# Performance work log

Hardware: AMD Instinct MI355X
Metric: run time of the kernel (lower is better)

Reference implementation:

```python
import jax, jax.numpy as jnp
import numpy as np

D = 512       # d_model
H = 8         # n_heads
L = 6         # n_blocks
DFF = 2048    # d_ffn
IN_DIM = 4096
OUT_DIM = 1000
B = 8
S = 512
DK = D // H
EPS = 1e-5
NEG = -1e9    # masked_fill value from source (-1000000000.0)

# sinusoidal positional encoding table (matches Positional_Encoding)
_pos = np.arange(5000)[:, None].astype(np.float64)
_div = np.exp(np.arange(0, D, 2) * (-np.log(10000.0) / D))
_pe = np.zeros((5000, D), np.float32)
_pe[:, 0::2] = np.sin(_pos * _div)
_pe[:, 1::2] = np.cos(_pos * _div)
PE = jnp.asarray(_pe)


def _ln(x, g, b):
    m = jnp.mean(x, -1, keepdims=True)
    v = jnp.var(x, -1, keepdims=True)
    return (x - m) * jax.lax.rsqrt(v + EPS) * g + b


def _attn(q, k, v, causal):
    # q:[B,Sq,D], k/v:[B,Sk,D] -> multi-head attention with source's quirky mask
    b, sq, _ = q.shape
    sk = k.shape[1]
    q = q.reshape(b, sq, H, DK).transpose(0, 2, 1, 3)
    k = k.reshape(b, sk, H, DK).transpose(0, 2, 1, 3)
    v = v.reshape(b, sk, H, DK).transpose(0, 2, 1, 3)
    s = jnp.einsum('bhqd,bhkd->bhqk', q, k) / jnp.sqrt(jnp.asarray(DK, q.dtype))
    mask = s != 0.0  # faithful: source masks positions where score == padding (0)
    if causal:
        mask = mask & jnp.tril(jnp.ones((sq, sk), bool))
    s = jnp.where(mask, s, NEG)
    p = jax.nn.softmax(s, axis=-1)
    o = jnp.einsum('bhqk,bhkd->bhqd', p, v)
    return o.transpose(0, 2, 1, 3).reshape(b, sq, D)


def _ffn(x, w1, b1, w2, b2):
    return jax.nn.relu(x @ w1 + b1) @ w2 + b2


def setup_inputs() -> dict:
    key = jax.random.key(0)
    ks = iter(jax.random.split(key, 40))

    def w(shape, s=0.02):
        return jax.random.normal(next(ks), shape, jnp.float32) * s

    inp = {}
    inp['x'] = jax.random.randint(next(ks), (B, S), 0, IN_DIM)
    inp['target'] = jax.random.randint(next(ks), (B,), 0, OUT_DIM)
    inp['in_emb'] = w((IN_DIM, D), 1.0)
    inp['out_emb'] = w((OUT_DIM, D), 1.0)
    # encoder params (stacked over layers)
    inp['enc_qkv_w'] = w((L, 3, D, D))
    inp['enc_qkv_b'] = w((L, 3, D))
    inp['enc_ln1_g'] = jnp.ones((L, D), jnp.float32)
    inp['enc_ln1_b'] = jnp.zeros((L, D), jnp.float32)
    inp['enc_ffn1_w'] = w((L, D, DFF))
    inp['enc_ffn1_b'] = w((L, DFF))
    inp['enc_ffn2_w'] = w((L, DFF, D))
    inp['enc_ffn2_b'] = w((L, D))
    inp['enc_ln2_g'] = jnp.ones((L, D), jnp.float32)
    inp['enc_ln2_b'] = jnp.zeros((L, D), jnp.float32)
    # decoder params
    inp['dec_qkv1_w'] = w((L, 3, D, D))
    inp['dec_qkv1_b'] = w((L, 3, D))
    inp['dec_ln1_g'] = jnp.ones((L, D), jnp.float32)
    inp['dec_ln1_b'] = jnp.zeros((L, D), jnp.float32)
    inp['dec_qkv2_w'] = w((L, 3, D, D))
    inp['dec_qkv2_b'] = w((L, 3, D))
    inp['dec_ln2_g'] = jnp.ones((L, D), jnp.float32)
    inp['dec_ln2_b'] = jnp.zeros((L, D), jnp.float32)
    inp['dec_ffn1_w'] = w((L, D, DFF))
    inp['dec_ffn1_b'] = w((L, DFF))
    inp['dec_ffn2_w'] = w((L, DFF, D))
    inp['dec_ffn2_b'] = w((L, D))
    inp['dec_ln3_g'] = jnp.ones((L, D), jnp.float32)
    inp['dec_ln3_b'] = jnp.zeros((L, D), jnp.float32)
    inp['out_w'] = w((D, OUT_DIM))
    inp['out_b'] = w((OUT_DIM,))
    return inp


def reference(x, target, in_emb, out_emb,
              enc_qkv_w, enc_qkv_b, enc_ln1_g, enc_ln1_b,
              enc_ffn1_w, enc_ffn1_b, enc_ffn2_w, enc_ffn2_b,
              enc_ln2_g, enc_ln2_b,
              dec_qkv1_w, dec_qkv1_b, dec_ln1_g, dec_ln1_b,
              dec_qkv2_w, dec_qkv2_b, dec_ln2_g, dec_ln2_b,
              dec_ffn1_w, dec_ffn1_b, dec_ffn2_w, dec_ffn2_b,
              dec_ln3_g, dec_ln3_b, out_w, out_b):
    scale = jnp.sqrt(jnp.float32(D))
    # encoder: embed tokens + positional encoding (dropout is identity at eval)
    e = in_emb[x] * scale + PE[None, :S]
    for i in range(L):
        q = e @ enc_qkv_w[i, 0] + enc_qkv_b[i, 0]
        k = e @ enc_qkv_w[i, 1] + enc_qkv_b[i, 1]
        v = e @ enc_qkv_w[i, 2] + enc_qkv_b[i, 2]
        e = _ln(_attn(q, k, v, False) + e, enc_ln1_g[i], enc_ln1_b[i])
        e = _ln(e + _ffn(e, enc_ffn1_w[i], enc_ffn1_b[i], enc_ffn2_w[i], enc_ffn2_b[i]),
                enc_ln2_g[i], enc_ln2_b[i])
    # decoder: target.unsqueeze(1) -> seq len 1
    d = out_emb[target][:, None, :] * scale + PE[None, :1]
    for i in range(L):
        q = d @ dec_qkv1_w[i, 0] + dec_qkv1_b[i, 0]
        k = d @ dec_qkv1_w[i, 1] + dec_qkv1_b[i, 1]
        v = d @ dec_qkv1_w[i, 2] + dec_qkv1_b[i, 2]
        d = _ln(_attn(q, k, v, True) + d, dec_ln1_g[i], dec_ln1_b[i])
        q = d @ dec_qkv2_w[i, 0] + dec_qkv2_b[i, 0]
        k = e @ dec_qkv2_w[i, 1] + dec_qkv2_b[i, 1]
        v = e @ dec_qkv2_w[i, 2] + dec_qkv2_b[i, 2]
        d = _ln(_attn(q, k, v, False) + d, dec_ln2_g[i], dec_ln2_b[i])
        d = _ln(d + _ffn(d, dec_ffn1_w[i], dec_ffn1_b[i], dec_ffn2_w[i], dec_ffn2_b[i]),
                dec_ln3_g[i], dec_ln3_b[i])
    return d @ out_w + out_b  # [B, 1, OUT_DIM] logits (source never applies its softmax)
```

## Files before the change

kernel.cpp:

```cpp
#include <hip/hip_runtime.h>
#include <hip/hip_bf16.h>

#define DM 512
#define NH 8
#define DK 64
#define SEQ 512
#define NB 8
#define NL 6
#define DFF 2048
#define OUTD 1000
#define EMB_SCALE 22.627416997969522f
#define PE_C (-0.017988946039015984)

typedef __bf16 bf16x8 __attribute__((ext_vector_type(8)));
typedef __bf16 bf16x4 __attribute__((ext_vector_type(4)));
typedef float f32x4 __attribute__((ext_vector_type(4)));

__device__ __forceinline__ void load16_lds(const __bf16* g, __bf16* l) {
  __builtin_amdgcn_global_load_lds(
      (const __attribute__((address_space(1))) void*)g,
      (__attribute__((address_space(3))) void*)l, 16, 0, 0);
}

__device__ __forceinline__ float dot8(bf16x8 w, const float* a) {
  float s = 0.f;
#pragma unroll
  for (int j = 0; j < 8; ++j) s += (float)w[j] * a[j];
  return s;
}

__global__ __launch_bounds__(256) void pe_kernel(float* __restrict__ pe) {
  int s = blockIdx.x;
  int d2 = threadIdx.x;
  double div = exp((double)(2 * d2) * PE_C);
  double arg = (double)s * div;
  pe[(size_t)s * DM + 2 * d2] = (float)sin(arg);
  pe[(size_t)s * DM + 2 * d2 + 1] = (float)cos(arg);
}

__global__ __launch_bounds__(256) void embed_enc(const int* __restrict__ x,
                                                 const float* __restrict__ emb,
                                                 const float* __restrict__ pe,
                                                 float* __restrict__ e,
                                                 __bf16* __restrict__ eb) {
  int idx = blockIdx.x * 256 + threadIdx.x;
  int d = idx & (DM - 1);
  int bs = idx >> 9;
  int s = bs & (SEQ - 1);
  int tok = x[bs];
  float v = emb[(size_t)tok * DM + d] * EMB_SCALE + pe[(size_t)s * DM + d];
  e[idx] = v;
  eb[idx] = (__bf16)v;
}

__global__ __launch_bounds__(256) void embed_dec(const int* __restrict__ t,
                                                 const float* __restrict__ emb,
                                                 float* __restrict__ dd) {
  int idx = blockIdx.x * 256 + threadIdx.x;
  int d = idx & (DM - 1);
  int b = idx >> 9;
  float pe = (d & 1) ? 1.0f : 0.0f;
  dd[idx] = emb[(size_t)t[b] * DM + d] * EMB_SCALE + pe;
}

__global__ __launch_bounds__(256) void transpose_w(const float* __restrict__ W,
                                                   __bf16* __restrict__ WT,
                                                   int K, int N) {
  __shared__ float t[32][33];
  size_t off = (size_t)blockIdx.z * K * N;
  W += off; WT += off;
  int k0 = blockIdx.y * 32, n0 = blockIdx.x * 32;
  int tx = threadIdx.x & 7, ty = threadIdx.x >> 3;
  float4 v = *(const float4*)&W[(size_t)(k0 + ty) * N + n0 + tx * 4];
  t[ty][tx * 4 + 0] = v.x; t[ty][tx * 4 + 1] = v.y;
  t[ty][tx * 4 + 2] = v.z; t[ty][tx * 4 + 3] = v.w;
  __syncthreads();
  bf16x4 o;
  o[0] = (__bf16)t[tx * 4 + 0][ty];
  o[1] = (__bf16)t[tx * 4 + 1][ty];
  o[2] = (__bf16)t[tx * 4 + 2][ty];
  o[3] = (__bf16)t[tx * 4 + 3][ty];
  *(bf16x4*)&WT[(size_t)(n0 + ty) * K + k0 + tx * 4] = o;
}

__global__ __launch_bounds__(256) void transpose_ow(const float* __restrict__ W,
                                                    __bf16* __restrict__ WT) {
  __shared__ float t[32][33];
  int n0 = blockIdx.x * 32, k0 = blockIdx.y * 32;
  int tid = threadIdx.x;
  for (int i = tid; i < 1024; i += 256) {
    int kk = i >> 5, nn = i & 31;
    t[kk][nn] = (n0 + nn < OUTD) ? W[(size_t)(k0 + kk) * OUTD + n0 + nn] : 0.f;
  }
  __syncthreads();
  for (int i = tid; i < 1024; i += 256) {
    int nn = i >> 5, kk = i & 31;
    if (n0 + nn < OUTD)
      WT[(size_t)(n0 + nn) * DM + k0 + kk] = (__bf16)t[kk][nn];
  }
}

template <int BN, bool RELU, bool WF32, bool WBF16, bool TRV, bool KVM>
__global__ __launch_bounds__(256) void mfma_gemm(
    const __bf16* __restrict__ A, const __bf16* __restrict__ BT,
    const float* __restrict__ bias, float* __restrict__ C,
    __bf16* __restrict__ Cb, __bf16* __restrict__ Vt, int M, int N, int K,
    long btStride, long bStride, long cStride) {
  int z = blockIdx.z;
  if (KVM) {
    long idx = (long)(z >> 1) * 3 + 1 + (z & 1);
    BT += idx * btStride;
    bias += idx * bStride;
  } else {
    BT += (size_t)z * btStride;
    bias += (size_t)z * bStride;
  }
  if (WF32) C += (size_t)z * cStride;
  if (WBF16) Cb += (size_t)z * cStride;

  constexpr int NI = BN / 32;
  __shared__ __bf16 As[128 * 64];
  __shared__ __bf16 Bs[BN * 64];

  int tid = threadIdx.x;
  int wave = tid >> 6, lane = tid & 63;
  int wm = wave >> 1, wn = wave & 1;
  int quad = lane >> 4, l16 = lane & 15;
  int rlane = lane >> 3, c8 = lane & 7;
  int m0 = blockIdx.y * 128, n0 = blockIdx.x * BN;
  int gcol = ((c8 ^ rlane) * 8);

  f32x4 acc[4][NI];
#pragma unroll
  for (int i = 0; i < 4; ++i)
#pragma unroll
    for (int j = 0; j < NI; ++j) acc[i][j] = (f32x4){0.f, 0.f, 0.f, 0.f};

  for (int k0 = 0; k0 < K; k0 += 64) {
    __syncthreads();
#pragma unroll
    for (int j = 0; j < 4; ++j) {
      int row = j * 32 + wave * 8 + rlane;
      load16_lds(&A[(size_t)(m0 + row) * K + k0 + gcol],
                 &As[(j * 32 + wave * 8) * 64]);
    }
#pragma unroll
    for (int j = 0; j < BN / 32; ++j) {
      int row = j * 32 + wave * 8 + rlane;
      load16_lds(&BT[(size_t)(n0 + row) * K + k0 + gcol],
                 &Bs[(j * 32 + wave * 8) * 64]);
    }
    __syncthreads();
#pragma unroll
    for (int kk = 0; kk < 64; kk += 32) {
      bf16x8 af[4], bf[NI];
#pragma unroll
      for (int i = 0; i < 4; ++i) {
        int row = wm * 64 + i * 16 + l16;
        af[i] = *(const bf16x8*)&As[row * 64 + ((((kk >> 3) + quad) ^ (row & 7)) * 8)];
      }
#pragma unroll
      for (int i = 0; i < NI; ++i) {
        int row = wn * (BN / 2) + i * 16 + l16;
        bf[i] = *(const bf16x8*)&Bs[row * 64 + ((((kk >> 3) + quad) ^ (row & 7)) * 8)];
      }
#pragma unroll
      for (int mi = 0; mi < 4; ++mi)
#pragma unroll
        for (int ni = 0; ni < NI; ++ni)
          acc[mi][ni] = __builtin_amdgcn_mfma_f32_16x16x32_bf16(
              af[mi], bf[ni], acc[mi][ni], 0, 0, 0);
    }
  }

#pragma unroll
  for (int ni = 0; ni < NI; ++ni) {
    int col = n0 + wn * (BN / 2) + ni * 16 + l16;
    float bv = bias[col];
    if (TRV && z == 2) {
      int b = m0 >> 9;
#pragma unroll
      for (int mi = 0; mi < 4; ++mi) {
        int srow = (m0 & 511) + wm * 64 + mi * 16 + quad * 4;
        bf16x4 pk;
#pragma unroll
        for (int r = 0; r < 4; ++r) pk[r] = (__bf16)(acc[mi][ni][r] + bv);
        *(bf16x4*)&Vt[((size_t)(b * 512 + col)) * 512 + srow] = pk;
      }
    } else {
#pragma unroll
      for (int mi = 0; mi < 4; ++mi) {
#pragma unroll
        for (int r = 0; r < 4; ++r) {
          int row = m0 + wm * 64 + mi * 16 + quad * 4 + r;
          float v = acc[mi][ni][r] + bv;
          if (RELU) v = fmaxf(v, 0.f);
          if (WF32) C[(size_t)row * N + col] = v;
          if (WBF16) Cb[(size_t)row * N + col] = (__bf16)v;
        }
      }
    }
  }
}

#define SCP 520
__global__ __launch_bounds__(256) void attn_mfma(const __bf16* __restrict__ QKV,
                                                 const __bf16* __restrict__ Vt,
                                                 float* __restrict__ O) {
  __shared__ __bf16 Sc[16 * SCP];
  __shared__ __bf16 Tt[64 * 64];

  const long ACTL = (long)NB * SEQ * DM;
  int tid = threadIdx.x;
  int wave = tid >> 6, lane = tid & 63;
  int quad = lane >> 4, l16 = lane & 15;
  int rlane = lane >> 3, c8 = lane & 7;
  int q0 = blockIdx.x * 16;
  int bh = blockIdx.y, b = bh >> 3, h = bh & 7;
  const __bf16* Q = QKV;
  const __bf16* Kp = QKV + ACTL;
  size_t baseQ = ((size_t)b * SEQ + q0) * DM + h * DK;
  size_t baseK = ((size_t)b * SEQ) * DM + h * DK;
  const __bf16* VtB = Vt + ((size_t)(b * 512 + h * 64)) * 512;
  int gcol = (c8 ^ rlane) * 8;

  bf16x8 af0 = *(const bf16x8*)&Q[baseQ + (size_t)l16 * DM + quad * 8];
  bf16x8 af1 = *(const bf16x8*)&Q[baseQ + (size_t)l16 * DM + 32 + quad * 8];

  for (int kt = 0; kt < 8; ++kt) {
    __syncthreads();
#pragma unroll
    for (int j = 0; j < 2; ++j) {
      int row = j * 32 + wave * 8 + rlane;
      load16_lds(&Kp[baseK + (size_t)(kt * 64 + row) * DM + gcol],
                 &Tt[(j * 32 + wave * 8) * 64]);
    }
    __syncthreads();
    f32x4 acc = (f32x4){0.f, 0.f, 0.f, 0.f};
    int krow = wave * 16 + l16, sw = krow & 7;
    bf16x8 b0 = *(const bf16x8*)&Tt[krow * 64 + ((quad ^ sw) * 8)];
    bf16x8 b1 = *(const bf16x8*)&Tt[krow * 64 + (((4 + quad) ^ sw) * 8)];
    acc = __builtin_amdgcn_mfma_f32_16x16x32_bf16(af0, b0, acc, 0, 0, 0);
    acc = __builtin_amdgcn_mfma_f32_16x16x32_bf16(af1, b1, acc, 0, 0, 0);
#pragma unroll
    for (int r = 0; r < 4; ++r)
      Sc[(quad * 4 + r) * SCP + kt * 64 + wave * 16 + l16] =
          (__bf16)(acc[r] * 0.125f);
  }
  __syncthreads();

#pragma unroll
  for (int rr = 0; rr < 4; ++rr) {
    int r = wave * 4 + rr;
    float v[8];
    float mx = -1e30f;
#pragma unroll
    for (int j = 0; j < 8; ++j) {
      v[j] = (float)Sc[r * SCP + j * 64 + lane];
      mx = fmaxf(mx, v[j]);
    }
    for (int o = 32; o > 0; o >>= 1) mx = fmaxf(mx, __shfl_xor(mx, o));
    float sum = 0.f;
#pragma unroll
    for (int j = 0; j < 8; ++j) { v[j] = __expf(v[j] - mx); sum += v[j]; }
    for (int o = 32; o > 0; o >>= 1) sum += __shfl_xor(sum, o);
    float inv = 1.f / sum;
#pragma unroll
    for (int j = 0; j < 8; ++j)
      Sc[r * SCP + j * 64 + lane] = (__bf16)(v[j] * inv);
  }

  f32x4 oacc = (f32x4){0.f, 0.f, 0.f, 0.f};
  for (int kt = 0; kt < 8; ++kt) {
    __syncthreads();
#pragma unroll
    for (int j = 0; j < 2; ++j) {
      int row = j * 32 + wave * 8 + rlane;
      load16_lds(&VtB[(size_t)row * 512 + kt * 64 + gcol],
                 &Tt[(j * 32 + wave * 8) * 64]);
    }
    __syncthreads();
    int drow = wave * 16 + l16, sw = drow & 7;
#pragma unroll
    for (int kk = 0; kk < 64; kk += 32) {
      bf16x8 pa = *(const bf16x8*)&Sc[l16 * SCP + kt * 64 + kk + quad * 8];
      bf16x8 vb = *(const bf16x8*)&Tt[drow * 64 + ((((kk >> 3) + quad) ^ sw) * 8)];
      oacc = __builtin_amdgcn_mfma_f32_16x16x32_bf16(pa, vb, oacc, 0, 0, 0);
    }
  }
#pragma unroll
  for (int r = 0; r < 4; ++r)
    O[((size_t)b * SEQ + q0 + quad * 4 + r) * DM + h * DK + wave * 16 + l16] =
        oacc[r];
}

template <bool WB>
__global__ __launch_bounds__(256) void add_ln(
    const float* __restrict__ x, const float* __restrict__ res,
    const float* __restrict__ cbias,
    const float* __restrict__ g, const float* __restrict__ beta,
    float* __restrict__ y, __bf16* __restrict__ yb) {
  int row = blockIdx.x;
  int tid = threadIdx.x;
  const float* xr = x + (size_t)row * DM;
  const float* rr = res + (size_t)row * DM;
  float b0 = cbias ? cbias[tid] : 0.f;
  float b1 = cbias ? cbias[tid + 256] : 0.f;
  float v0 = xr[tid] + b0 + rr[tid];
  float v1 = xr[tid + 256] + b1 + rr[tid + 256];
  float s = v0 + v1, sq = v0 * v0 + v1 * v1;
  for (int o = 32; o > 0; o >>= 1) {
    s += __shfl_xor(s, o);
    sq += __shfl_xor(sq, o);
  }
  __shared__ float ps[4], pq[4];
  int wv = tid >> 6;
  if ((tid & 63) == 0) { ps[wv] = s; pq[wv] = sq; }
  __syncthreads();
  s = ps[0] + ps[1] + ps[2] + ps[3];
  sq = pq[0] + pq[1] + pq[2] + pq[3];
  float mean = s * (1.f / DM);
  float var = sq * (1.f / DM) - mean * mean;
  float rstd = rsqrtf(var + 1e-5f);
  float o0 = (v0 - mean) * rstd * g[tid] + beta[tid];
  float o1 = (v1 - mean) * rstd * g[tid + 256] + beta[tid + 256];
  y[(size_t)row * DM + tid] = o0;
  y[(size_t)row * DM + tid + 256] = o1;
  if (WB) {
    yb[(size_t)row * DM + tid] = (__bf16)o0;
    yb[(size_t)row * DM + tid + 256] = (__bf16)o1;
  }
}


__global__ __launch_bounds__(256) void dec_vln(
    float* __restrict__ dd, const __bf16* __restrict__ WvT,
    const float* __restrict__ bv, const float* __restrict__ g,
    const float* __restrict__ beta) {
  __shared__ float arow[DM];
  int r = blockIdx.x, tid = threadIdx.x;
  arow[tid] = dd[(size_t)r * DM + tid];
  arow[tid + 256] = dd[(size_t)r * DM + tid + 256];
  __syncthreads();
  float out[2];
#pragma unroll
  for (int cc = 0; cc < 2; ++cc) {
    int c = tid + cc * 256;
    const __bf16* w = &WvT[(size_t)c * DM];
    float acc = 0.f;
#pragma unroll 4
    for (int k = 0; k < DM; k += 8) acc += dot8(*(const bf16x8*)&w[k], &arow[k]);
    out[cc] = arow[c] + acc + bv[c];
  }
  float s = out[0] + out[1], sq = out[0] * out[0] + out[1] * out[1];
  for (int o = 32; o > 0; o >>= 1) { s += __shfl_xor(s, o); sq += __shfl_xor(sq, o); }
  __shared__ float ps[4], pq[4];
  int wv = tid >> 6;
  if ((tid & 63) == 0) { ps[wv] = s; pq[wv] = sq; }
  __syncthreads();
  s = ps[0] + ps[1] + ps[2] + ps[3];
  sq = pq[0] + pq[1] + pq[2] + pq[3];
  float mean = s * (1.f / DM);
  float rstd = rsqrtf(sq * (1.f / DM) - mean * mean + 1e-5f);
  dd[(size_t)r * DM + tid] = (out[0] - mean) * rstd * g[tid] + beta[tid];
  dd[(size_t)r * DM + tid + 256] = (out[1] - mean) * rstd * g[tid + 256] + beta[tid + 256];
}

__global__ __launch_bounds__(256) void dec_qattn(
    const float* __restrict__ dd, const __bf16* __restrict__ WqT,
    const float* __restrict__ qb, const __bf16* __restrict__ Kb,
    const __bf16* __restrict__ Vb, float* __restrict__ da) {
  __shared__ float arow[DM];
  __shared__ float red[4][64];
  __shared__ float q[64];
  __shared__ float sc[SEQ];
  __shared__ float wred[4];
  __shared__ float smax, ssum;

  int bh = blockIdx.x, b = bh >> 3, h = bh & 7;
  int tid = threadIdx.x, lane = tid & 63, wave = tid >> 6;
  arow[tid] = dd[(size_t)b * DM + tid];
  arow[tid + 256] = dd[(size_t)b * DM + tid + 256];
  __syncthreads();

  {
    int c = tid & 63, s = tid >> 6;
    const __bf16* w = &WqT[(size_t)(h * 64 + c) * DM + s * 128];
    float acc = 0.f;
#pragma unroll
    for (int k = 0; k < 128; k += 8) acc += dot8(*(const bf16x8*)&w[k], &arow[s * 128 + k]);
    red[s][c] = acc;
  }
  __syncthreads();
  if (tid < 64) q[tid] = red[0][tid] + red[1][tid] + red[2][tid] + red[3][tid] + qb[h * 64 + tid];
  __syncthreads();

  for (int key = tid; key < SEQ; key += 256) {
    const __bf16* kp = &Kb[((size_t)b * SEQ + key) * DM + h * 64];
    float acc = 0.f;
#pragma unroll
    for (int k = 0; k < 64; k += 8) acc += dot8(*(const bf16x8*)&kp[k], &q[k]);
    sc[key] = acc * 0.125f;
  }
  __syncthreads();
  float m = -1e30f;
  for (int j = tid; j < SEQ; j += 256) m = fmaxf(m, sc[j]);
  for (int o = 32; o > 0; o >>= 1) m = fmaxf(m, __shfl_xor(m, o));
  if (lane == 0) wred[wave] = m;
  __syncthreads();
  m = fmaxf(fmaxf(wred[0], wred[1]), fmaxf(wred[2], wred[3]));
  float sum = 0.f;
  for (int j = tid; j < SEQ; j += 256) {
    float p = __expf(sc[j] - m);
    sc[j] = p;
    sum += p;
  }
  for (int o = 32; o > 0; o >>= 1) sum += __shfl_xor(sum, o);
  __syncthreads();
  if (lane == 0) wred[wave] = sum;
  __syncthreads();
  float inv = 1.f / (wred[0] + wred[1] + wred[2] + wred[3]);

  {
    int d = tid & 63, s = tid >> 6;
    float acc = 0.f;
    const __bf16* vp = &Vb[((size_t)b * SEQ + s * 128) * DM + h * 64 + d];
#pragma unroll 8
    for (int k = 0; k < 128; ++k) acc += sc[s * 128 + k] * (float)vp[(size_t)k * DM];
    red[s][d] = acc;
  }
  __syncthreads();
  if (tid < 64)
    da[(size_t)b * DM + h * 64 + tid] =
        (red[0][tid] + red[1][tid] + red[2][tid] + red[3][tid]) * inv;
}

__global__ __launch_bounds__(256) void dec_ffn1(
    const float* __restrict__ dd, const __bf16* __restrict__ W1T,
    const float* __restrict__ b1, float* __restrict__ h) {
  __shared__ float a[8][DM];
  int tid = threadIdx.x, lane = tid & 63, wave = tid >> 6;
  for (int i = tid; i < 8 * DM; i += 256) a[i >> 9][i & 511] = dd[i];
  __syncthreads();
  int col = blockIdx.x * 4 + wave;
  bf16x8 w = *(const bf16x8*)&W1T[(size_t)col * DM + lane * 8];
  float acc[8];
#pragma unroll
  for (int r = 0; r < 8; ++r) acc[r] = dot8(w, &a[r][lane * 8]);
#pragma unroll
  for (int r = 0; r < 8; ++r)
    for (int o = 32; o > 0; o >>= 1) acc[r] += __shfl_xor(acc[r], o);
  if (lane == 0) {
    float bb = b1[col];
#pragma unroll
    for (int r = 0; r < 8; ++r) h[(size_t)r * DFF + col] = fmaxf(acc[r] + bb, 0.f);
  }
}

__global__ __launch_bounds__(256) void dec_ffn2(
    const float* __restrict__ h, const __bf16* __restrict__ W2T,
    const float* __restrict__ b2, float* __restrict__ df) {
  __shared__ float red[4][8];
  int tid = threadIdx.x, lane = tid & 63, wave = tid >> 6;
  int c = wave >> 1, half = wave & 1;
  int col = blockIdx.x * 2 + c;
  int k0 = half * 1024 + lane * 8;
  bf16x8 w0 = *(const bf16x8*)&W2T[(size_t)col * DFF + k0];
  bf16x8 w1 = *(const bf16x8*)&W2T[(size_t)col * DFF + k0 + 512];
  float acc[8];
#pragma unroll
  for (int r = 0; r < 8; ++r) {
    float4 h0a = *(const float4*)&h[(size_t)r * DFF + k0];
    float4 h0b = *(const float4*)&h[(size_t)r * DFF + k0 + 4];
    float4 h1a = *(const float4*)&h[(size_t)r * DFF + k0 + 512];
    float4 h1b = *(const float4*)&h[(size_t)r * DFF + k0 + 516];
    float hh0[8] = {h0a.x, h0a.y, h0a.z, h0a.w, h0b.x, h0b.y, h0b.z, h0b.w};
    float hh1[8] = {h1a.x, h1a.y, h1a.z, h1a.w, h1b.x, h1b.y, h1b.z, h1b.w};
    acc[r] = dot8(w0, hh0) + dot8(w1, hh1);
  }
#pragma unroll
  for (int r = 0; r < 8; ++r)
    for (int o = 32; o > 0; o >>= 1) acc[r] += __shfl_xor(acc[r], o);
  if (lane == 0) {
#pragma unroll
    for (int r = 0; r < 8; ++r) red[wave][r] = acc[r];
  }
  __syncthreads();
  if (tid < 16) {
    int cc = tid >> 3, r = tid & 7;
    int ocol = blockIdx.x * 2 + cc;
    df[(size_t)r * DM + ocol] =
        red[cc * 2][r] + red[cc * 2 + 1][r] + b2[ocol];
  }
}

__global__ __launch_bounds__(256) void dec_out(
    const float* __restrict__ dd, const __bf16* __restrict__ WoT,
    const float* __restrict__ ob, float* __restrict__ out) {
  __shared__ float a[8][DM];
  int tid = threadIdx.x, lane = tid & 63, wave = tid >> 6;
  for (int i = tid; i < 8 * DM; i += 256) a[i >> 9][i & 511] = dd[i];
  __syncthreads();
  int col = blockIdx.x * 4 + wave;
  bf16x8 w = *(const bf16x8*)&WoT[(size_t)col * DM + lane * 8];
  float acc[8];
#pragma unroll
  for (int r = 0; r < 8; ++r) acc[r] = dot8(w, &a[r][lane * 8]);
#pragma unroll
  for (int r = 0; r < 8; ++r)
    for (int o = 32; o > 0; o >>= 1) acc[r] += __shfl_xor(acc[r], o);
  if (lane == 0) {
    float bb = ob[col];
#pragma unroll
    for (int r = 0; r < 8; ++r) out[(size_t)r * OUTD + col] = acc[r] + bb;
  }
}

extern "C" void kernel_launch(void* const* d_in, const int* in_sizes, int n_in,
                              void* d_out, int out_size, void* d_ws, size_t ws_size,
                              hipStream_t stream) {
  const int* x = (const int*)d_in[0];
  const int* target = (const int*)d_in[1];
  const float* in_emb = (const float*)d_in[2];
  const float* out_emb = (const float*)d_in[3];
  const float* enc_qkv_w = (const float*)d_in[4];
  const float* enc_qkv_b = (const float*)d_in[5];
  const float* enc_ln1_g = (const float*)d_in[6];
  const float* enc_ln1_b = (const float*)d_in[7];
  const float* enc_ffn1_w = (const float*)d_in[8];
  const float* enc_ffn1_b = (const float*)d_in[9];
  const float* enc_ffn2_w = (const float*)d_in[10];
  const float* enc_ffn2_b = (const float*)d_in[11];
  const float* enc_ln2_g = (const float*)d_in[12];
  const float* enc_ln2_b = (const float*)d_in[13];
  const float* dec_qkv1_w = (const float*)d_in[14];
  const float* dec_qkv1_b = (const float*)d_in[15];
  const float* dec_ln1_g = (const float*)d_in[16];
  const float* dec_ln1_b = (const float*)d_in[17];
  const float* dec_qkv2_w = (const float*)d_in[18];
  const float* dec_qkv2_b = (const float*)d_in[19];
  const float* dec_ln2_g = (const float*)d_in[20];
  const float* dec_ln2_b = (const float*)d_in[21];
  const float* dec_ffn1_w = (const float*)d_in[22];
  const float* dec_ffn1_b = (const float*)d_in[23];
  const float* dec_ffn2_w = (const float*)d_in[24];
  const float* dec_ffn2_b = (const float*)d_in[25];
  const float* dec_ln3_g = (const float*)d_in[26];
  const float* dec_ln3_b = (const float*)d_in[27];
  const float* out_w = (const float*)d_in[28];
  const float* out_b = (const float*)d_in[29];

  const long ACTL = (long)NB * SEQ * DM;
  const int M = NB * SEQ;
  const long WQS = (long)DM * DM;
  const long WFS = (long)DM * DFF;

  char* p = (char*)d_ws;
  float* e = (float*)p;            p += ACTL * 4;
  float* tb = (float*)p;           p += ACTL * 4;
  float* pe = (float*)p;           p += (long)SEQ * DM * 4;
  float* dd = (float*)p;           p += NB * DM * 4;
  float* da = (float*)p;           p += NB * DM * 4;
  float* dh = (float*)p;           p += NB * DFF * 4;
  float* df = (float*)p;           p += NB * DM * 4;
  p = (char*)(((uintptr_t)p + 255) & ~(uintptr_t)255);
  __bf16* eb = (__bf16*)p;         p += ACTL * 2;
  __bf16* qkvb = (__bf16*)p;       p += 3 * ACTL * 2;
  __bf16* hbb = (__bf16*)p;        p += (long)M * DFF * 2;
  __bf16* kvb = (__bf16*)p;        p += 12L * ACTL * 2;
  __bf16* wtq = (__bf16*)p;        p += 18L * WQS * 2;
  __bf16* wtf1 = (__bf16*)p;       p += 6L * WFS * 2;
  __bf16* wtf2 = (__bf16*)p;       p += 6L * WFS * 2;
  __bf16* wtd = (__bf16*)p;        p += 18L * WQS * 2;
  __bf16* wtd1 = (__bf16*)p;       p += 18L * WQS * 2;
  __bf16* wf1t = (__bf16*)p;       p += 6L * WFS * 2;
  __bf16* wf2t = (__bf16*)p;       p += 6L * WFS * 2;
  __bf16* wot = (__bf16*)p;        p += (long)OUTD * DM * 2;

  __bf16* vtb = qkvb + 2 * ACTL;

  pe_kernel<<<SEQ, 256, 0, stream>>>(pe);
  transpose_w<<<dim3(16, 16, 18), 256, 0, stream>>>(enc_qkv_w, wtq, DM, DM);
  transpose_w<<<dim3(64, 16, 6), 256, 0, stream>>>(enc_ffn1_w, wtf1, DM, DFF);
  transpose_w<<<dim3(16, 64, 6), 256, 0, stream>>>(enc_ffn2_w, wtf2, DFF, DM);
  transpose_w<<<dim3(16, 16, 18), 256, 0, stream>>>(dec_qkv2_w, wtd, DM, DM);
  transpose_w<<<dim3(16, 16, 18), 256, 0, stream>>>(dec_qkv1_w, wtd1, DM, DM);
  transpose_w<<<dim3(64, 16, 6), 256, 0, stream>>>(dec_ffn1_w, wf1t, DM, DFF);
  transpose_w<<<dim3(16, 64, 6), 256, 0, stream>>>(dec_ffn2_w, wf2t, DFF, DM);
  transpose_ow<<<dim3(32, 16), 256, 0, stream>>>(out_w, wot);

  embed_enc<<<(M * DM) / 256, 256, 0, stream>>>(x, in_emb, pe, e, eb);
  for (int i = 0; i < NL; ++i) {
    mfma_gemm<128, false, false, true, true, false><<<dim3(4, 32, 3), 256, 0, stream>>>(
        eb, wtq + (size_t)i * 3 * WQS, enc_qkv_b + (size_t)i * 3 * DM,
        nullptr, qkvb, vtb, M, DM, DM, WQS, DM, ACTL);
    attn_mfma<<<dim3(SEQ / 16, NB * NH), 256, 0, stream>>>(qkvb, vtb, tb);
    add_ln<true><<<M, 256, 0, stream>>>(tb, e, nullptr, enc_ln1_g + i * DM,
                                        enc_ln1_b + i * DM, e, eb);
    mfma_gemm<128, true, false, true, false, false><<<dim3(16, 32, 1), 256, 0, stream>>>(
        eb, wtf1 + (size_t)i * WFS, enc_ffn1_b + (size_t)i * DFF,
        nullptr, hbb, nullptr, M, DFF, DM, 0, 0, 0);
    mfma_gemm<64, false, true, false, false, false><<<dim3(8, 32, 1), 256, 0, stream>>>(
        hbb, wtf2 + (size_t)i * WFS, enc_ffn2_b + (size_t)i * DM,
        tb, nullptr, nullptr, M, DM, DFF, 0, 0, 0);
    add_ln<true><<<M, 256, 0, stream>>>(tb, e, nullptr, enc_ln2_g + i * DM,
                                        enc_ln2_b + i * DM, e, eb);
  }

  mfma_gemm<128, false, false, true, false, true><<<dim3(4, 32, 12), 256, 0, stream>>>(
      eb, wtd, dec_qkv2_b, nullptr, kvb, nullptr, M, DM, DM, WQS, DM, ACTL);

  embed_dec<<<(NB * DM) / 256, 256, 0, stream>>>(target, out_emb, dd);
  for (int i = 0; i < NL; ++i) {
    dec_vln<<<8, 256, 0, stream>>>(
        dd, wtd1 + ((size_t)i * 3 + 2) * WQS, dec_qkv1_b + ((size_t)i * 3 + 2) * DM,
        dec_ln1_g + i * DM, dec_ln1_b + i * DM);
    dec_qattn<<<64, 256, 0, stream>>>(
        dd, wtd + (size_t)i * 3 * WQS, dec_qkv2_b + (size_t)i * 3 * DM,
        kvb + (size_t)i * 2 * ACTL, kvb + ((size_t)i * 2 + 1) * ACTL, da);
    add_ln<false><<<NB, 256, 0, stream>>>(
        da, dd, nullptr, dec_ln2_g + i * DM, dec_ln2_b + i * DM, dd, nullptr);
    dec_ffn1<<<DFF / 4, 256, 0, stream>>>(
        dd, wf1t + (size_t)i * WFS, dec_ffn1_b + (size_t)i * DFF, dh);
    dec_ffn2<<<DM / 2, 256, 0, stream>>>(
        dh, wf2t + (size_t)i * WFS, dec_ffn2_b + (size_t)i * DM, df);
    add_ln<false><<<NB, 256, 0, stream>>>(
        df, dd, nullptr, dec_ln3_g + i * DM, dec_ln3_b + i * DM, dd, nullptr);
  }

  dec_out<<<OUTD / 4, 256, 0, stream>>>(dd, wot, out_b, (float*)d_out);
}
```

Before: 1.234 ms.

## Fuse decoder into persistent grid-barrier megakernel reading fp32 weights directly

New measurement: 1.544 ms. 25.2% more time.

```diff
diff --git a/kernel.cpp b/kernel.cpp
--- a/kernel.cpp
+++ b/kernel.cpp
@@ -10,7 +10,7 @@
 #define DFF 2048
 #define OUTD 1000
 #define EMB_SCALE 22.627416997969522f
-#define PE_C (-0.017988946039015984)
+#define PE_C (-0.017988946039015984f)
 
 typedef __bf16 bf16x8 __attribute__((ext_vector_type(8)));
 typedef __bf16 bf16x4 __attribute__((ext_vector_type(4)));
@@ -29,18 +29,8 @@
   return s;
 }
 
-__global__ __launch_bounds__(256) void pe_kernel(float* __restrict__ pe) {
-  int s = blockIdx.x;
-  int d2 = threadIdx.x;
-  double div = exp((double)(2 * d2) * PE_C);
-  double arg = (double)s * div;
-  pe[(size_t)s * DM + 2 * d2] = (float)sin(arg);
-  pe[(size_t)s * DM + 2 * d2 + 1] = (float)cos(arg);
-}
-
 __global__ __launch_bounds__(256) void embed_enc(const int* __restrict__ x,
                                                  const float* __restrict__ emb,
-                                                 const float* __restrict__ pe,
                                                  float* __restrict__ e,
                                                  __bf16* __restrict__ eb) {
   int idx = blockIdx.x * 256 + threadIdx.x;
@@ -48,19 +38,12 @@
   int bs = idx >> 9;
   int s = bs & (SEQ - 1);
   int tok = x[bs];
-  float v = emb[(size_t)tok * DM + d] * EMB_SCALE + pe[(size_t)s * DM + d];
+  float div = __expf((float)(d & ~1) * PE_C);
+  float arg = (float)s * div;
+  float pe = (d & 1) ? cosf(arg) : sinf(arg);
+  float v = emb[(size_t)tok * DM + d] * EMB_SCALE + pe;
   e[idx] = v;
   eb[idx] = (__bf16)v;
-}
-
-__global__ __launch_bounds__(256) void embed_dec(const int* __restrict__ t,
-                                                 const float* __restrict__ emb,
-                                                 float* __restrict__ dd) {
-  int idx = blockIdx.x * 256 + threadIdx.x;
-  int d = idx & (DM - 1);
-  int b = idx >> 9;
-  float pe = (d & 1) ? 1.0f : 0.0f;
-  dd[idx] = emb[(size_t)t[b] * DM + d] * EMB_SCALE + pe;
 }
 
 __global__ __launch_bounds__(256) void transpose_w(const float* __restrict__ W,
@@ -83,23 +66,6 @@
   *(bf16x4*)&WT[(size_t)(n0 + ty) * K + k0 + tx * 4] = o;
 }
 
-__global__ __launch_bounds__(256) void transpose_ow(const float* __restrict__ W,
-                                                    __bf16* __restrict__ WT) {
-  __shared__ float t[32][33];
-  int n0 = blockIdx.x * 32, k0 = blockIdx.y * 32;
-  int tid = threadIdx.x;
-  for (int i = tid; i < 1024; i += 256) {
-    int kk = i >> 5, nn = i & 31;
-    t[kk][nn] = (n0 + nn < OUTD) ? W[(size_t)(k0 + kk) * OUTD + n0 + nn] : 0.f;
-  }
-  __syncthreads();
-  for (int i = tid; i < 1024; i += 256) {
-    int nn = i >> 5, kk = i & 31;
-    if (n0 + nn < OUTD)
-      WT[(size_t)(n0 + nn) * DM + k0 + kk] = (__bf16)t[kk][nn];
-  }
-}
-
 template <int BN, bool RELU, bool WF32, bool WBF16, bool TRV, bool KVM>
 __global__ __launch_bounds__(256) void mfma_gemm(
     const __bf16* __restrict__ A, const __bf16* __restrict__ BT,
@@ -297,17 +263,14 @@
 template <bool WB>
 __global__ __launch_bounds__(256) void add_ln(
     const float* __restrict__ x, const float* __restrict__ res,
-    const float* __restrict__ cbias,
     const float* __restrict__ g, const float* __restrict__ beta,
     float* __restrict__ y, __bf16* __restrict__ yb) {
   int row = blockIdx.x;
   int tid = threadIdx.x;
   const float* xr = x + (size_t)row * DM;
   const float* rr = res + (size_t)row * DM;
-  float b0 = cbias ? cbias[tid] : 0.f;
-  float b1 = cbias ? cbias[tid + 256] : 0.f;
-  float v0 = xr[tid] + b0 + rr[tid];
-  float v1 = xr[tid + 256] + b1 + rr[tid + 256];
+  float v0 = xr[tid] + rr[tid];
+  float v1 = xr[tid + 256] + rr[tid + 256];
   float s = v0 + v1, sq = v0 * v0 + v1 * v1;
   for (int o = 32; o > 0; o >>= 1) {
     s += __shfl_xor(s, o);
@@ -332,29 +295,38 @@
   }
 }
 
-
-__global__ __launch_bounds__(256) void dec_vln(
-    float* __restrict__ dd, const __bf16* __restrict__ WvT,
-    const float* __restrict__ bv, const float* __restrict__ g,
-    const float* __restrict__ beta) {
-  __shared__ float arow[DM];
-  int r = blockIdx.x, tid = threadIdx.x;
-  arow[tid] = dd[(size_t)r * DM + tid];
-  arow[tid + 256] = dd[(size_t)r * DM + tid + 256];
+#define DBLK 64
+#define WQS_ 262144L
+#define WFS_ 1048576L
+#define ACTL_ 2097152L
+
+__device__ __forceinline__ void gridbar(unsigned* cnt, unsigned target) {
   __syncthreads();
-  float out[2];
-#pragma unroll
-  for (int cc = 0; cc < 2; ++cc) {
-    int c = tid + cc * 256;
-    const __bf16* w = &WvT[(size_t)c * DM];
-    float acc = 0.f;
-#pragma unroll 4
-    for (int k = 0; k < DM; k += 8) acc += dot8(*(const bf16x8*)&w[k], &arow[k]);
-    out[cc] = arow[c] + acc + bv[c];
-  }
-  float s = out[0] + out[1], sq = out[0] * out[0] + out[1] * out[1];
-  for (int o = 32; o > 0; o >>= 1) { s += __shfl_xor(s, o); sq += __shfl_xor(sq, o); }
+  if (threadIdx.x == 0) {
+    __threadfence();
+    __hip_atomic_fetch_add(cnt, 1u, __ATOMIC_RELEASE, __HIP_MEMORY_SCOPE_AGENT);
+    while (__hip_atomic_load(cnt, __ATOMIC_ACQUIRE, __HIP_MEMORY_SCOPE_AGENT) <
+           target)
+      __builtin_amdgcn_s_sleep(2);
+    __threadfence();
+  }
+  __syncthreads();
+}
+
+__device__ __forceinline__ void ln_row256(const float* __restrict__ x,
+                                          const float* __restrict__ res,
+                                          const float* __restrict__ g,
+                                          const float* __restrict__ beta,
+                                          float* __restrict__ y) {
   __shared__ float ps[4], pq[4];
+  int tid = threadIdx.x;
+  float v0 = x[tid] + res[tid];
+  float v1 = x[tid + 256] + res[tid + 256];
+  float s = v0 + v1, sq = v0 * v0 + v1 * v1;
+  for (int o = 32; o > 0; o >>= 1) {
+    s += __shfl_xor(s, o);
+    sq += __shfl_xor(sq, o);
+  }
   int wv = tid >> 6;
   if ((tid & 63) == 0) { ps[wv] = s; pq[wv] = sq; }
   __syncthreads();
@@ -362,157 +334,186 @@
   sq = pq[0] + pq[1] + pq[2] + pq[3];
   float mean = s * (1.f / DM);
   float rstd = rsqrtf(sq * (1.f / DM) - mean * mean + 1e-5f);
-  dd[(size_t)r * DM + tid] = (out[0] - mean) * rstd * g[tid] + beta[tid];
-  dd[(size_t)r * DM + tid + 256] = (out[1] - mean) * rstd * g[tid + 256] + beta[tid + 256];
-}
-
-__global__ __launch_bounds__(256) void dec_qattn(
-    const float* __restrict__ dd, const __bf16* __restrict__ WqT,
-    const float* __restrict__ qb, const __bf16* __restrict__ Kb,
-    const __bf16* __restrict__ Vb, float* __restrict__ da) {
-  __shared__ float arow[DM];
+  y[tid] = (v0 - mean) * rstd * g[tid] + beta[tid];
+  y[tid + 256] = (v1 - mean) * rstd * g[tid + 256] + beta[tid + 256];
+}
+
+__global__ __launch_bounds__(256) void zero_u32(unsigned* p) {
+  if (threadIdx.x == 0) *p = 0u;
+}
+
+__global__ __launch_bounds__(256) void dec_mega(
+    const int* __restrict__ tgt, const float* __restrict__ out_emb,
+    const float* __restrict__ qkv1_w, const float* __restrict__ qkv1_b,
+    const float* __restrict__ ln1_g, const float* __restrict__ ln1_b,
+    const float* __restrict__ qkv2_w, const float* __restrict__ qkv2_b,
+    const float* __restrict__ ln2_g, const float* __restrict__ ln2_b,
+    const float* __restrict__ ffn1_w, const float* __restrict__ ffn1_b,
+    const float* __restrict__ ffn2_w, const float* __restrict__ ffn2_b,
+    const float* __restrict__ ln3_g, const float* __restrict__ ln3_b,
+    const float* __restrict__ ow, const float* __restrict__ ob,
+    const __bf16* __restrict__ kvb,
+    float* __restrict__ dd, float* __restrict__ t1, float* __restrict__ qv,
+    float* __restrict__ da, float* __restrict__ dh,
+    unsigned* __restrict__ cnt, float* __restrict__ out) {
   __shared__ float red[4][64];
   __shared__ float q[64];
-  __shared__ float sc[SEQ];
+  __shared__ float sc[512];
   __shared__ float wred[4];
-  __shared__ float smax, ssum;
-
-  int bh = blockIdx.x, b = bh >> 3, h = bh & 7;
-  int tid = threadIdx.x, lane = tid & 63, wave = tid >> 6;
-  arow[tid] = dd[(size_t)b * DM + tid];
-  arow[tid + 256] = dd[(size_t)b * DM + tid + 256];
-  __syncthreads();
-
-  {
-    int c = tid & 63, s = tid >> 6;
-    const __bf16* w = &WqT[(size_t)(h * 64 + c) * DM + s * 128];
-    float acc = 0.f;
-#pragma unroll
-    for (int k = 0; k < 128; k += 8) acc += dot8(*(const bf16x8*)&w[k], &arow[s * 128 + k]);
-    red[s][c] = acc;
-  }
-  __syncthreads();
-  if (tid < 64) q[tid] = red[0][tid] + red[1][tid] + red[2][tid] + red[3][tid] + qb[h * 64 + tid];
-  __syncthreads();
-
-  for (int key = tid; key < SEQ; key += 256) {
-    const __bf16* kp = &Kb[((size_t)b * SEQ + key) * DM + h * 64];
-    float acc = 0.f;
-#pragma unroll
-    for (int k = 0; k < 64; k += 8) acc += dot8(*(const bf16x8*)&kp[k], &q[k]);
-    sc[key] = acc * 0.125f;
-  }
-  __syncthreads();
-  float m = -1e30f;
-  for (int j = tid; j < SEQ; j += 256) m = fmaxf(m, sc[j]);
-  for (int o = 32; o > 0; o >>= 1) m = fmaxf(m, __shfl_xor(m, o));
-  if (lane == 0) wred[wave] = m;
-  __syncthreads();
-  m = fmaxf(fmaxf(wred[0], wred[1]), fmaxf(wred[2], wred[3]));
-  float sum = 0.f;
-  for (int j = tid; j < SEQ; j += 256) {
-    float p = __expf(sc[j] - m);
-    sc[j] = p;
-    sum += p;
-  }
-  for (int o = 32; o > 0; o >>= 1) sum += __shfl_xor(sum, o);
-  __syncthreads();
-  if (lane == 0) wred[wave] = sum;
-  __syncthreads();
-  float inv = 1.f / (wred[0] + wred[1] + wred[2] + wred[3]);
-
-  {
-    int d = tid & 63, s = tid >> 6;
-    float acc = 0.f;
-    const __bf16* vp = &Vb[((size_t)b * SEQ + s * 128) * DM + h * 64 + d];
+
+  int tid = threadIdx.x, blk = blockIdx.x;
+  int gid = blk * 256 + tid;
+  unsigned phase = 0;
+
+  if (gid < NB * DM) {
+    int b = gid >> 9, d = gid & 511;
+    dd[gid] = out_emb[(size_t)tgt[b] * DM + d] * EMB_SCALE + ((d & 1) ? 1.f : 0.f);
+  }
+  gridbar(cnt, ++phase * DBLK);
+
+  for (int i = 0; i < NL; ++i) {
+    {
+      const float* Wv = qkv1_w + ((size_t)i * 3 + 2) * WQS_;
+      const float* bv = qkv1_b + ((size_t)i * 3 + 2) * DM;
+      int o = blk * 64 + (tid & 63);
+      int b = o >> 9, c = o & 511, ks = tid >> 6;
+      const float* ar = dd + b * 512;
+      float a0 = 0.f, a1 = 0.f;
+      for (int k = ks * 128; k < ks * 128 + 128; k += 2) {
+        a0 += ar[k] * Wv[(size_t)k * 512 + c];
+        a1 += ar[k + 1] * Wv[(size_t)(k + 1) * 512 + c];
+      }
+      red[ks][tid & 63] = a0 + a1;
+      __syncthreads();
+      if (tid < 64) {
+        int o2 = blk * 64 + tid;
+        t1[o2] = red[0][tid] + red[1][tid] + red[2][tid] + red[3][tid] +
+                 bv[o2 & 511];
+      }
+    }
+    gridbar(cnt, ++phase * DBLK);
+    if (blk < NB)
+      ln_row256(t1 + blk * 512, dd + blk * 512, ln1_g + i * DM, ln1_b + i * DM,
+                dd + blk * 512);
+    gridbar(cnt, ++phase * DBLK);
+
+    {
+      const float* Wq = qkv2_w + (size_t)i * 3 * WQS_;
+      const float* bq = qkv2_b + (size_t)i * 3 * DM;
+      int o = blk * 64 + (tid & 63);
+      int b = o >> 9, c = o & 511, ks = tid >> 6;
+      const float* ar = dd + b * 512;
+      float a0 = 0.f, a1 = 0.f;
+      for (int k = ks * 128; k < ks * 128 + 128; k += 2) {
+        a0 += ar[k] * Wq[(size_t)k * 512 + c];
+        a1 += ar[k + 1] * Wq[(size_t)(k + 1) * 512 + c];
+      }
+      red[ks][tid & 63] = a0 + a1;
+      __syncthreads();
+      if (tid < 64) {
+        int o2 = blk * 64 + tid;
+        qv[o2] = red[0][tid] + red[1][tid] + red[2][tid] + red[3][tid] +
+                 bq[o2 & 511];
+      }
+    }
+    gridbar(cnt, ++phase * DBLK);
+
+    {
+      int b = blk >> 3, h = blk & 7;
+      int lane = tid & 63, wave = tid >> 6;
+      const __bf16* Kb = kvb + (size_t)i * 2 * ACTL_;
+      const __bf16* Vb = Kb + ACTL_;
+      if (tid < 64) q[tid] = qv[b * 512 + h * 64 + tid];
+      __syncthreads();
+      for (int key = tid; key < 512; key += 256) {
+        const __bf16* kp = &Kb[((size_t)b * 512 + key) * 512 + h * 64];
+        float acc = 0.f;
+#pragma unroll
+        for (int k = 0; k < 64; k += 8) acc += dot8(*(const bf16x8*)&kp[k], &q[k]);
+        sc[key] = acc * 0.125f;
+      }
+      __syncthreads();
+      float m = -1e30f;
+      for (int j = tid; j < 512; j += 256) m = fmaxf(m, sc[j]);
+      for (int o = 32; o > 0; o >>= 1) m = fmaxf(m, __shfl_xor(m, o));
+      if (lane == 0) wred[wave] = m;
+      __syncthreads();
+      m = fmaxf(fmaxf(wred[0], wred[1]), fmaxf(wred[2], wred[3]));
+      float sum = 0.f;
+      for (int j = tid; j < 512; j += 256) {
+        float pv = __expf(sc[j] - m);
+        sc[j] = pv;
+        sum += pv;
+      }
+      for (int o = 32; o > 0; o >>= 1) sum += __shfl_xor(sum, o);
+      __syncthreads();
+      if (lane == 0) wred[wave] = sum;
+      __syncthreads();
+      float inv = 1.f / (wred[0] + wred[1] + wred[2] + wred[3]);
+      int d = tid & 63, s4 = tid >> 6;
+      float acc = 0.f;
+      const __bf16* vp = &Vb[((size_t)b * 512 + s4 * 128) * 512 + h * 64 + d];
 #pragma unroll 8
-    for (int k = 0; k < 128; ++k) acc += sc[s * 128 + k] * (float)vp[(size_t)k * DM];
-    red[s][d] = acc;
-  }
-  __syncthreads();
-  if (tid < 64)
-    da[(size_t)b * DM + h * 64 + tid] =
-        (red[0][tid] + red[1][tid] + red[2][tid] + red[3][tid]) * inv;
-}
-
-__global__ __launch_bounds__(256) void dec_ffn1(
-    const float* __restrict__ dd, const __bf16* __restrict__ W1T,
-    const float* __restrict__ b1, float* __restrict__ h) {
-  __shared__ float a[8][DM];
-  int tid = threadIdx.x, lane = tid & 63, wave = tid >> 6;
-  for (int i = tid; i < 8 * DM; i += 256) a[i >> 9][i & 511] = dd[i];
-  __syncthreads();
-  int col = blockIdx.x * 4 + wave;
-  bf16x8 w = *(const bf16x8*)&W1T[(size_t)col * DM + lane * 8];
-  float acc[8];
-#pragma unroll
-  for (int r = 0; r < 8; ++r) acc[r] = dot8(w, &a[r][lane * 8]);
-#pragma unroll
-  for (int r = 0; r < 8; ++r)
-    for (int o = 32; o > 0; o >>= 1) acc[r] += __shfl_xor(acc[r], o);
-  if (lane == 0) {
-    float bb = b1[col];
-#pragma unroll
-    for (int r = 0; r < 8; ++r) h[(size_t)r * DFF + col] = fmaxf(acc[r] + bb, 0.f);
-  }
-}
-
-__global__ __launch_bounds__(256) void dec_ffn2(
-    const float* __restrict__ h, const __bf16* __restrict__ W2T,
-    const float* __restrict__ b2, float* __restrict__ df) {
-  __shared__ float red[4][8];
-  int tid = threadIdx.x, lane = tid & 63, wave = tid >> 6;
-  int c = wave >> 1, half = wave & 1;
-  int col = blockIdx.x * 2 + c;
-  int k0 = half * 1024 + lane * 8;
-  bf16x8 w0 = *(const bf16x8*)&W2T[(size_t)col * DFF + k0];
-  bf16x8 w1 = *(const bf16x8*)&W2T[(size_t)col * DFF + k0 + 512];
-  float acc[8];
-#pragma unroll
-  for (int r = 0; r < 8; ++r) {
-    float4 h0a = *(const float4*)&h[(size_t)r * DFF + k0];
-    float4 h0b = *(const float4*)&h[(size_t)r * DFF + k0 + 4];
-    float4 h1a = *(const float4*)&h[(size_t)r * DFF + k0 + 512];
-    float4 h1b = *(const float4*)&h[(size_t)r * DFF + k0 + 516];
-    float hh0[8] = {h0a.x, h0a.y, h0a.z, h0a.w, h0b.x, h0b.y, h0b.z, h0b.w};
-    float hh1[8] = {h1a.x, h1a.y, h1a.z, h1a.w, h1b.x, h1b.y, h1b.z, h1b.w};
-    acc[r] = dot8(w0, hh0) + dot8(w1, hh1);
-  }
-#pragma unroll
-  for (int r = 0; r < 8; ++r)
-    for (int o = 32; o > 0; o >>= 1) acc[r] += __shfl_xor(acc[r], o);
-  if (lane == 0) {
-#pragma unroll
-    for (int r = 0; r < 8; ++r) red[wave][r] = acc[r];
-  }
-  __syncthreads();
-  if (tid < 16) {
-    int cc = tid >> 3, r = tid & 7;
-    int ocol = blockIdx.x * 2 + cc;
-    df[(size_t)r * DM + ocol] =
-        red[cc * 2][r] + red[cc * 2 + 1][r] + b2[ocol];
-  }
-}
-
-__global__ __launch_bounds__(256) void dec_out(
-    const float* __restrict__ dd, const __bf16* __restrict__ WoT,
-    const float* __restrict__ ob, float* __restrict__ out) {
-  __shared__ float a[8][DM];
-  int tid = threadIdx.x, lane = tid & 63, wave = tid >> 6;
-  for (int i = tid; i < 8 * DM; i += 256) a[i >> 9][i & 511] = dd[i];
-  __syncthreads();
-  int col = blockIdx.x * 4 + wave;
-  bf16x8 w = *(const bf16x8*)&WoT[(size_t)col * DM + lane * 8];
-  float acc[8];
-#pragma unroll
-  for (int r = 0; r < 8; ++r) acc[r] = dot8(w, &a[r][lane * 8]);
-#pragma unroll
-  for (int r = 0; r < 8; ++r)
-    for (int o = 32; o > 0; o >>= 1) acc[r] += __shfl_xor(acc[r], o);
-  if (lane == 0) {
-    float bb = ob[col];
-#pragma unroll
-    for (int r = 0; r < 8; ++r) out[(size_t)r * OUTD + col] = acc[r] + bb;
+      for (int k = 0; k < 128; ++k) acc += sc[s4 * 128 + k] * (float)vp[(size_t)k * 512];
+      red[s4][d] = acc;
+      __syncthreads();
+      if (tid < 64)
+        da[b * 512 + h * 64 + tid] =
+            (red[0][tid] + red[1][tid] + red[2][tid] + red[3][tid]) * inv;
+    }
+    gridbar(cnt, ++phase * DBLK);
+    if (blk < NB)
+      ln_row256(da + blk * 512, dd + blk * 512, ln2_g + i * DM, ln2_b + i * DM,
+                dd + blk * 512);
+    gridbar(cnt, ++phase * DBLK);
+
+    {
+      const float* W1 = ffn1_w + (size_t)i * WFS_;
+      int b = gid >> 11, c = gid & 2047;
+      const float* ar = dd + b * 512;
+      float a0 = 0.f, a1 = 0.f;
+      for (int k = 0; k < 512; k += 2) {
+        a0 += ar[k] * W1[(size_t)k * 2048 + c];
+        a1 += ar[k + 1] * W1[(size_t)(k + 1) * 2048 + c];
+      }
+      dh[gid] = fmaxf(a0 + a1 + ffn1_b[i * DFF + c], 0.f);
+    }
+    gridbar(cnt, ++phase * DBLK);
+
+    {
+      const float* W2 = ffn2_w + (size_t)i * WFS_;
+      int o = blk * 64 + (tid & 63);
+      int b = o >> 9, c = o & 511, ks = tid >> 6;
+      const float* hr = dh + b * 2048;
+      float a0 = 0.f, a1 = 0.f;
+      for (int k = ks * 512; k < ks * 512 + 512; k += 2) {
+        a0 += hr[k] * W2[(size_t)k * 512 + c];
+        a1 += hr[k + 1] * W2[(size_t)(k + 1) * 512 + c];
+      }
+      red[ks][tid & 63] = a0 + a1;
+      __syncthreads();
+      if (tid < 64) {
+        int o2 = blk * 64 + tid;
+        t1[o2] = red[0][tid] + red[1][tid] + red[2][tid] + red[3][tid] +
+                 ffn2_b[i * DM + (o2 & 511)];
+      }
+    }
+    gridbar(cnt, ++phase * DBLK);
+    if (blk < NB)
+      ln_row256(t1 + blk * 512, dd + blk * 512, ln3_g + i * DM, ln3_b + i * DM,
+                dd + blk * 512);
+    gridbar(cnt, ++phase * DBLK);
+  }
+
+  if (gid < NB * OUTD) {
+    int b = gid / OUTD, c = gid - b * OUTD;
+    const float* ar = dd + b * 512;
+    float a0 = 0.f, a1 = 0.f;
+    for (int k = 0; k < 512; k += 2) {
+      a0 += ar[k] * ow[(size_t)k * OUTD + c];
+      a1 += ar[k + 1] * ow[(size_t)(k + 1) * OUTD + c];
+    }
+    out[gid] = a0 + a1 + ob[c];
   }
 }
 
@@ -558,11 +559,12 @@
   char* p = (char*)d_ws;
   float* e = (float*)p;            p += ACTL * 4;
   float* tb = (float*)p;           p += ACTL * 4;
-  float* pe = (float*)p;           p += (long)SEQ * DM * 4;
   float* dd = (float*)p;           p += NB * DM * 4;
+  float* t1 = (float*)p;           p += NB * DM * 4;
+  float* qv = (float*)p;           p += NB * DM * 4;
   float* da = (float*)p;           p += NB * DM * 4;
   float* dh = (float*)p;           p += NB * DFF * 4;
-  float* df = (float*)p;           p += NB * DM * 4;
+  unsigned* cnt = (unsigned*)p;    p += 256;
   p = (char*)(((uintptr_t)p + 255) & ~(uintptr_t)255);
   __bf16* eb = (__bf16*)p;         p += ACTL * 2;
   __bf16* qkvb = (__bf16*)p;       p += 3 * ACTL * 2;
@@ -572,30 +574,22 @@
   __bf16* wtf1 = (__bf16*)p;       p += 6L * WFS * 2;
   __bf16* wtf2 = (__bf16*)p;       p += 6L * WFS * 2;
   __bf16* wtd = (__bf16*)p;        p += 18L * WQS * 2;
-  __bf16* wtd1 = (__bf16*)p;       p += 18L * WQS * 2;
-  __bf16* wf1t = (__bf16*)p;       p += 6L * WFS * 2;
-  __bf16* wf2t = (__bf16*)p;       p += 6L * WFS * 2;
-  __bf16* wot = (__bf16*)p;        p += (long)OUTD * DM * 2;
 
   __bf16* vtb = qkvb + 2 * ACTL;
 
-  pe_kernel<<<SEQ, 256, 0, stream>>>(pe);
   transpose_w<<<dim3(16, 16, 18), 256, 0, stream>>>(enc_qkv_w, wtq, DM, DM);
   transpose_w<<<dim3(64, 16, 6), 256, 0, stream>>>(enc_ffn1_w, wtf1, DM, DFF);
   transpose_w<<<dim3(16, 64, 6), 256, 0, stream>>>(enc_ffn2_w, wtf2, DFF, DM);
   transpose_w<<<dim3(16, 16, 18), 256, 0, stream>>>(dec_qkv2_w, wtd, DM, DM);
-  transpose_w<<<dim3(16, 16, 18), 256, 0, stream>>>(dec_qkv1_w, wtd1, DM, DM);
-  transpose_w<<<dim3(64, 16, 6), 256, 0, stream>>>(dec_ffn1_w, wf1t, DM, DFF);
-  transpose_w<<<dim3(16, 64, 6), 256, 0, stream>>>(dec_ffn2_w, wf2t, DFF, DM);
-  transpose_ow<<<dim3(32, 16), 256, 0, stream>>>(out_w, wot);
-
-  embed_enc<<<(M * DM) / 256, 256, 0, stream>>>(x, in_emb, pe, e, eb);
+  zero_u32<<<1, 256, 0, stream>>>(cnt);
+
+  embed_enc<<<(M * DM) / 256, 256, 0, stream>>>(x, in_emb, e, eb);
   for (int i = 0; i < NL; ++i) {
     mfma_gemm<128, false, false, true, true, false><<<dim3(4, 32, 3), 256, 0, stream>>>(
         eb, wtq + (size_t)i * 3 * WQS, enc_qkv_b + (size_t)i * 3 * DM,
         nullptr, qkvb, vtb, M, DM, DM, WQS, DM, ACTL);
     attn_mfma<<<dim3(SEQ / 16, NB * NH), 256, 0, stream>>>(qkvb, vtb, tb);
-    add_ln<true><<<M, 256, 0, stream>>>(tb, e, nullptr, enc_ln1_g + i * DM,
+    add_ln<true><<<M, 256, 0, stream>>>(tb, e, enc_ln1_g + i * DM,
                                         enc_ln1_b + i * DM, e, eb);
     mfma_gemm<128, true, false, true, false, false><<<dim3(16, 32, 1), 256, 0, stream>>>(
         eb, wtf1 + (size_t)i * WFS, enc_ffn1_b + (size_t)i * DFF,
@@ -603,30 +597,16 @@
     mfma_gemm<64, false, true, false, false, false><<<dim3(8, 32, 1), 256, 0, stream>>>(
         hbb, wtf2 + (size_t)i * WFS, enc_ffn2_b + (size_t)i * DM,
         tb, nullptr, nullptr, M, DM, DFF, 0, 0, 0);
-    add_ln<true><<<M, 256, 0, stream>>>(tb, e, nullptr, enc_ln2_g + i * DM,
+    add_ln<true><<<M, 256, 0, stream>>>(tb, e, enc_ln2_g + i * DM,
                                         enc_ln2_b + i * DM, e, eb);
   }
 
   mfma_gemm<128, false, false, true, false, true><<<dim3(4, 32, 12), 256, 0, stream>>>(
       eb, wtd, dec_qkv2_b, nullptr, kvb, nullptr, M, DM, DM, WQS, DM, ACTL);
 
-  embed_dec<<<(NB * DM) / 256, 256, 0, stream>>>(target, out_emb, dd);
-  for (int i = 0; i < NL; ++i) {
-    dec_vln<<<8, 256, 0, stream>>>(
-        dd, wtd1 + ((size_t)i * 3 + 2) * WQS, dec_qkv1_b + ((size_t)i * 3 + 2) * DM,
-        dec_ln1_g + i * DM, dec_ln1_b + i * DM);
-    dec_qattn<<<64, 256, 0, stream>>>(
-        dd, wtd + (size_t)i * 3 * WQS, dec_qkv2_b + (size_t)i * 3 * DM,
-        kvb + (size_t)i * 2 * ACTL, kvb + ((size_t)i * 2 + 1) * ACTL, da);
-    add_ln<false><<<NB, 256, 0, stream>>>(
-        da, dd, nullptr, dec_ln2_g + i * DM, dec_ln2_b + i * DM, dd, nullptr);
-    dec_ffn1<<<DFF / 4, 256, 0, stream>>>(
-        dd, wf1t + (size_t)i * WFS, dec_ffn1_b + (size_t)i * DFF, dh);
-    dec_ffn2<<<DM / 2, 256, 0, stream>>>(
-        dh, wf2t + (size_t)i * WFS, dec_ffn2_b + (size_t)i * DM, df);
-    add_ln<false><<<NB, 256, 0, stream>>>(
-        df, dd, nullptr, dec_ln3_g + i * DM, dec_ln3_b + i * DM, dd, nullptr);
-  }
-
-  dec_out<<<OUTD / 4, 256, 0, stream>>>(dd, wot, out_b, (float*)d_out);
-}
+  dec_mega<<<DBLK, 256, 0, stream>>>(
+      target, out_emb, dec_qkv1_w, dec_qkv1_b, dec_ln1_g, dec_ln1_b,
+      dec_qkv2_w, dec_qkv2_b, dec_ln2_g, dec_ln2_b, dec_ffn1_w, dec_ffn1_b,
+      dec_ffn2_w, dec_ffn2_b, dec_ln3_g, dec_ln3_b, out_w, out_b, kvb,
+      dd, t1, qv, da, dh, cnt, (float*)d_out);
+}
```
